# Kernel optimization log

Hardware: AMD Instinct MI355X
Metric: run time of the kernel (lower is better)

The kernel has to match this reference:

```python
import jax, jax.numpy as jnp
import numpy as np

B, S, DD, DE, DA = 32, 2048, 1024, 1024, 1024
NEG = -1000000000.0


def setup_inputs() -> dict:
    key = jax.random.key(0)
    k1, k2, k3, k4, k5 = jax.random.split(key, 5)
    query_state = jax.random.normal(k1, (B, DD), dtype=jnp.float32)
    encoder_hidden_states = jax.random.normal(k2, (B, S, DE), dtype=jnp.float32)
    attention_mask = jax.random.randint(k3, (B, S), 0, 2, dtype=jnp.int32)
    # W_c: Linear(DD+DE -> DA, bias=False): weight shape [DA, DD+DE]
    W_c = jax.random.normal(k4, (DA, DD + DE), dtype=jnp.float32) / np.sqrt(DD + DE)
    # V: Linear(DA -> 1, bias=False): weight shape [1, DA]
    V = jax.random.normal(k5, (1, DA), dtype=jnp.float32) / np.sqrt(DA)
    return {
        "query_state": query_state,
        "encoder_hidden_states": encoder_hidden_states,
        "attention_mask": attention_mask,
        "W_c": W_c,
        "V": V,
    }


def reference(query_state, encoder_hidden_states, attention_mask, W_c, V):
    # Split W_c along input dim: cat([q, e]) @ W_c.T == q @ Wq.T + e @ We.T
    Wq = W_c[:, :DD]          # [DA, DD]
    We = W_c[:, DD:]          # [DA, DE]
    q_proj = jnp.einsum('bd,ad->ba', query_state, Wq)            # [B, DA]
    e_proj = jnp.einsum('bsd,ad->bsa', encoder_hidden_states, We)  # [B, S, DA]
    energies = jnp.tanh(q_proj[:, None, :] + e_proj)             # [B, S, DA]
    scores = jnp.einsum('bsa,a->bs', energies, V[0])             # [B, S]
    scores = jnp.where(attention_mask == 0, NEG, scores)
    attention_weights = jax.nn.softmax(scores, axis=1)           # [B, S]
    context_vector = jnp.einsum('bs,bsd->bd', attention_weights, encoder_hidden_states)
    return context_vector, attention_weights
```

## Files before the change

kernel.cpp:

```cpp
#include <hip/hip_runtime.h>
#include <hip/hip_bf16.h>

#define NB 32
#define NS 2048
#define NDD 1024
#define NDE 1024
#define NDA 1024
#define NEGV (-1000000000.0f)

typedef __attribute__((ext_vector_type(8))) __bf16 bf16x8;
typedef __attribute__((ext_vector_type(4))) float f32x4;

__device__ __forceinline__ float fast_tanh(float x) {
    x = fminf(10.0f, fmaxf(-10.0f, x));
    float e = __expf(2.0f * x);
    return __fdividef(e - 1.0f, e + 1.0f);
}

__device__ __forceinline__ float bfu2f(unsigned short v) {
    union { unsigned u; float f; } c; c.u = (unsigned)v << 16; return c.f;
}

__global__ void prep_we(const float* __restrict__ Wc, __bf16* __restrict__ We) {
    int f = blockIdx.x * 256 + threadIdx.x;
    int a  = f >> 8;
    int k4 = f & 255;
    float4 v = *reinterpret_cast<const float4*>(Wc + (size_t)a * (NDD + NDE) + NDD + k4 * 4);
    union { __bf16 h[4]; uint2 u; } pk;
    pk.h[0] = (__bf16)v.x; pk.h[1] = (__bf16)v.y;
    pk.h[2] = (__bf16)v.z; pk.h[3] = (__bf16)v.w;
    *reinterpret_cast<uint2*>(We + (size_t)a * NDE + k4 * 4) = pk.u;
}

__global__ void prep_e(const float* __restrict__ E, __bf16* __restrict__ Eb) {
    size_t i = ((size_t)blockIdx.x * 256 + threadIdx.x) * 8;
    f32x4 x = __builtin_nontemporal_load(reinterpret_cast<const f32x4*>(E + i));
    f32x4 y = __builtin_nontemporal_load(reinterpret_cast<const f32x4*>(E + i + 4));
    union { __bf16 h[8]; uint4 u; } pk;
    pk.h[0] = (__bf16)x[0]; pk.h[1] = (__bf16)x[1]; pk.h[2] = (__bf16)x[2]; pk.h[3] = (__bf16)x[3];
    pk.h[4] = (__bf16)y[0]; pk.h[5] = (__bf16)y[1]; pk.h[6] = (__bf16)y[2]; pk.h[7] = (__bf16)y[3];
    *reinterpret_cast<uint4*>(Eb + i) = pk.u;
}

__global__ void qproj_kernel(const float* __restrict__ q, const float* __restrict__ Wc,
                             float* __restrict__ qp) {
    __shared__ float qs[NDD];
    int b = blockIdx.y;
    int a = blockIdx.x * 256 + threadIdx.x;
    float4 qv = *reinterpret_cast<const float4*>(q + (size_t)b * NDD + threadIdx.x * 4);
    *reinterpret_cast<float4*>(qs + threadIdx.x * 4) = qv;
    __syncthreads();
    const float* wrow = Wc + (size_t)a * (NDD + NDE);
    float acc = 0.f;
#pragma unroll 4
    for (int k4 = 0; k4 < 256; ++k4) {
        float4 w = *reinterpret_cast<const float4*>(wrow + k4 * 4);
        acc += qs[k4*4+0] * w.x + qs[k4*4+1] * w.y + qs[k4*4+2] * w.z + qs[k4*4+3] * w.w;
    }
    qp[(size_t)b * NDA + a] = acc;
}

__global__ __launch_bounds__(1024, 1) void score256(
    const __bf16* __restrict__ Eb, const __bf16* __restrict__ We,
    const float* __restrict__ qp, const float* __restrict__ Vv,
    float* __restrict__ sp) {
    __shared__ __align__(16) __bf16 As[2][256 * 64];
    __shared__ __align__(16) __bf16 Bs[2][256 * 64];

    const int tid  = threadIdx.x;
    const int lane = tid & 63;
    const int l15  = lane & 15;
    const int h    = lane >> 4;
    const int wid  = tid >> 6;
    const int wr   = wid >> 2;
    const int wc   = wid & 3;

    const int bid = blockIdx.x;
    const int xcd = bid & 7;
    const int j   = bid >> 3;
    const int m   = xcd * 32 + (j >> 2);
    const int n   = j & 3;
    const int row0  = m * 256;
    const int ncol0 = n * 256;
    const int b     = m >> 3;

    f32x4 acc[4][4];
#pragma unroll
    for (int mf = 0; mf < 4; ++mf)
#pragma unroll
        for (int nf = 0; nf < 4; ++nf)
            acc[mf][nf] = (f32x4){0.f, 0.f, 0.f, 0.f};

    int offE[2], offW[2];
#pragma unroll
    for (int i = 0; i < 2; ++i) {
        int chunk = i * 1024 + tid;
        int r  = chunk >> 3;
        int sg = (chunk & 7) ^ (r & 7);
        offE[i] = (row0  + r) * 1024 + sg * 8;
        offW[i] = (ncol0 + r) * 1024 + sg * 8;
    }

    const int slot0 = ((h ^ (l15 & 7)) * 16);
    const int aoffl = (wr * 64 + l15) * 128 + slot0;
    const int boffl = (wc * 64 + l15) * 128 + slot0;

#define STAGE4(abuf, bbuf, kc)                                                          \
    {                                                                                   \
        _Pragma("unroll")                                                               \
        for (int i = 0; i < 2; ++i)                                                     \
            __builtin_amdgcn_global_load_lds(                                           \
                (const __attribute__((address_space(1))) unsigned*)(Eb + offE[i] + (kc)),\
                (__attribute__((address_space(3))) unsigned*)((char*)(abuf) + i * 16384 + wid * 1024), \
                16, 0, 0);                                                              \
        _Pragma("unroll")                                                               \
        for (int i = 0; i < 2; ++i)                                                     \
            __builtin_amdgcn_global_load_lds(                                           \
                (const __attribute__((address_space(1))) unsigned*)(We + offW[i] + (kc)),\
                (__attribute__((address_space(3))) unsigned*)((char*)(bbuf) + i * 16384 + wid * 1024), \
                16, 0, 0);                                                              \
    }

    STAGE4(&As[0][0], &Bs[0][0], 0)
    float qv[4], vv[4];
#pragma unroll
    for (int nf = 0; nf < 4; ++nf) {
        int col = ncol0 + wc * 64 + nf * 16 + l15;
        qv[nf] = qp[(size_t)b * NDA + col];
        vv[nf] = Vv[col];
    }
    __syncthreads();

    for (int T = 0; T < 16; ++T) {
        const int cur = T & 1;
        const char* Ab = (const char*)&As[cur][0];
        const char* Bb = (const char*)&Bs[cur][0];
        if (T < 15) STAGE4(&As[cur ^ 1][0], &Bs[cur ^ 1][0], (T + 1) * 64)

#pragma unroll
        for (int ks = 0; ks < 2; ++ks) {
            bf16x8 bfr[4], afr[4];
#pragma unroll
            for (int nf = 0; nf < 4; ++nf)
                bfr[nf] = *reinterpret_cast<const bf16x8*>(Bb + ((boffl + nf * 2048) ^ (ks * 64)));
#pragma unroll
            for (int mf = 0; mf < 4; ++mf)
                afr[mf] = *reinterpret_cast<const bf16x8*>(Ab + ((aoffl + mf * 2048) ^ (ks * 64)));
            __builtin_amdgcn_s_setprio(1);
#pragma unroll
            for (int mf = 0; mf < 4; ++mf)
#pragma unroll
                for (int nf = 0; nf < 4; ++nf)
                    acc[mf][nf] = __builtin_amdgcn_mfma_f32_16x16x32_bf16(afr[mf], bfr[nf], acc[mf][nf], 0, 0, 0);
            __builtin_amdgcn_s_setprio(0);
        }
        __syncthreads();
    }

    float* ps2 = reinterpret_cast<float*>(&As[0][0]);
#pragma unroll
    for (int mf = 0; mf < 4; ++mf)
#pragma unroll
        for (int jj = 0; jj < 4; ++jj) {
            float s = 0.f;
#pragma unroll
            for (int nf = 0; nf < 4; ++nf)
                s += fast_tanh(qv[nf] + acc[mf][nf][jj]) * vv[nf];
            s += __shfl_xor(s, 1);
            s += __shfl_xor(s, 2);
            s += __shfl_xor(s, 4);
            s += __shfl_xor(s, 8);
            if (l15 == 0)
                ps2[(wr * 64 + mf * 16 + h * 4 + jj) * 4 + wc] = s;
        }
    __syncthreads();
    if (tid < 256)
        sp[(size_t)n * (NB * NS) + row0 + tid] =
            ps2[tid * 4] + ps2[tid * 4 + 1] + ps2[tid * 4 + 2] + ps2[tid * 4 + 3];
}

__global__ void softmax_kernel(const float* __restrict__ sp, const int* __restrict__ mask,
                               float* __restrict__ wout, int np) {
    int b = blockIdx.x;
    const int* mrow = mask + (size_t)b * NS;
    float v[8];
    float lmax = -INFINITY;
#pragma unroll
    for (int jj = 0; jj < 8; ++jj) {
        int s = threadIdx.x + 256 * jj;
        float sc = 0.f;
        for (int nn = 0; nn < np; ++nn) sc += sp[(size_t)nn * (NB * NS) + b * NS + s];
        v[jj] = (mrow[s] == 0) ? NEGV : sc;
        lmax = fmaxf(lmax, v[jj]);
    }
#pragma unroll
    for (int mm = 1; mm <= 32; mm <<= 1) lmax = fmaxf(lmax, __shfl_xor(lmax, mm));
    __shared__ float redm[4], reds[4];
    if ((threadIdx.x & 63) == 0) redm[threadIdx.x >> 6] = lmax;
    __syncthreads();
    float bmax = fmaxf(fmaxf(redm[0], redm[1]), fmaxf(redm[2], redm[3]));
    float lsum = 0.f;
#pragma unroll
    for (int jj = 0; jj < 8; ++jj) { v[jj] = __expf(v[jj] - bmax); lsum += v[jj]; }
#pragma unroll
    for (int mm = 1; mm <= 32; mm <<= 1) lsum += __shfl_xor(lsum, mm);
    if ((threadIdx.x & 63) == 0) reds[threadIdx.x >> 6] = lsum;
    __syncthreads();
    float inv = __fdividef(1.0f, reds[0] + reds[1] + reds[2] + reds[3]);
#pragma unroll
    for (int jj = 0; jj < 8; ++jj) wout[(size_t)b * NS + threadIdx.x + 256 * jj] = v[jj] * inv;
}

__global__ void context_bf16(const __bf16* __restrict__ Eb, const float* __restrict__ w,
                             float* __restrict__ ctx) {
    int b  = blockIdx.x >> 3;
    int dc = blockIdx.x & 7;
    int dg = threadIdx.x & 31;
    int ss = threadIdx.x >> 5;
    const __bf16* base = Eb + (size_t)b * NS * NDE + (size_t)(ss * 256) * NDE + dc * 128 + dg * 4;
    const float* wb = w + (size_t)b * NS + ss * 256;
    float a0 = 0.f, a1 = 0.f, a2 = 0.f, a3 = 0.f;
#pragma unroll 8
    for (int s = 0; s < 256; ++s) {
        float ws = wb[s];
        uint2 u = *reinterpret_cast<const uint2*>(base + (size_t)s * NDE);
        a0 = fmaf(ws, bfu2f((unsigned short)(u.x & 0xffff)), a0);
        a1 = fmaf(ws, bfu2f((unsigned short)(u.x >> 16)), a1);
        a2 = fmaf(ws, bfu2f((unsigned short)(u.y & 0xffff)), a2);
        a3 = fmaf(ws, bfu2f((unsigned short)(u.y >> 16)), a3);
    }
    __shared__ float4 part[256];
    part[threadIdx.x] = make_float4(a0, a1, a2, a3);
    __syncthreads();
    if (threadIdx.x < 32) {
        float4 r = part[threadIdx.x];
#pragma unroll
        for (int k = 1; k < 8; ++k) {
            float4 p = part[threadIdx.x + 32 * k];
            r.x += p.x; r.y += p.y; r.z += p.z; r.w += p.w;
        }
        *reinterpret_cast<float4*>(ctx + (size_t)b * NDD + dc * 128 + threadIdx.x * 4) = r;
    }
}

extern "C" void kernel_launch(void* const* d_in, const int* in_sizes, int n_in,
                              void* d_out, int out_size, void* d_ws, size_t ws_size,
                              hipStream_t stream) {
    const float* query = (const float*)d_in[0];
    const float* enc   = (const float*)d_in[1];
    const int*   mask  = (const int*)d_in[2];
    const float* Wc    = (const float*)d_in[3];
    const float* V     = (const float*)d_in[4];

    float* out = (float*)d_out;
    float* ctx = out;
    float* wts = out + NB * NDD;

    const size_t WE_B = (size_t)NDA * NDE * 2;
    const size_t QP_B = (size_t)NB * NDA * 4;
    const size_t SP_B = (size_t)8 * NB * NS * 4;
    char* ws = (char*)d_ws;
    __bf16* We = (__bf16*)ws;
    float*  qp = (float*)(ws + WE_B);
    float*  sp = (float*)(ws + WE_B + QP_B);
    __bf16* Eb = (__bf16*)(ws + WE_B + QP_B + SP_B);

    hipLaunchKernelGGL(prep_we,      dim3(1024),  dim3(256), 0, stream, Wc, We);
    hipLaunchKernelGGL(qproj_kernel, dim3(4, NB), dim3(256), 0, stream, query, Wc, qp);
    hipLaunchKernelGGL(prep_e,       dim3(32768), dim3(256), 0, stream, enc, Eb);
    hipLaunchKernelGGL(score256,     dim3(1024),  dim3(1024), 0, stream, Eb, We, qp, V, sp);
    hipLaunchKernelGGL(softmax_kernel, dim3(NB),  dim3(256), 0, stream, sp, mask, wts, 4);
    hipLaunchKernelGGL(context_bf16, dim3(256),   dim3(256), 0, stream, Eb, wts, ctx);
}
```

Before: 289.6 us.

## Halve K-tile to 32 and allow two 1024-thread blocks per CU

```diff
diff --git a/kernel.cpp b/kernel.cpp
--- a/kernel.cpp
+++ b/kernel.cpp
@@ -60,12 +60,12 @@
     qp[(size_t)b * NDA + a] = acc;
 }
 
-__global__ __launch_bounds__(1024, 1) void score256(
+__global__ __launch_bounds__(1024, 2) void score256(
     const __bf16* __restrict__ Eb, const __bf16* __restrict__ We,
     const float* __restrict__ qp, const float* __restrict__ Vv,
     float* __restrict__ sp) {
-    __shared__ __align__(16) __bf16 As[2][256 * 64];
-    __shared__ __align__(16) __bf16 Bs[2][256 * 64];
+    __shared__ __align__(16) __bf16 As[2][256 * 32];
+    __shared__ __align__(16) __bf16 Bs[2][256 * 32];
 
     const int tid  = threadIdx.x;
     const int lane = tid & 63;
@@ -91,37 +91,36 @@
         for (int nf = 0; nf < 4; ++nf)
             acc[mf][nf] = (f32x4){0.f, 0.f, 0.f, 0.f};
 
-    int offE[2], offW[2];
-#pragma unroll
-    for (int i = 0; i < 2; ++i) {
-        int chunk = i * 1024 + tid;
-        int r  = chunk >> 3;
-        int sg = (chunk & 7) ^ (r & 7);
-        offE[i] = (row0  + r) * 1024 + sg * 8;
-        offW[i] = (ncol0 + r) * 1024 + sg * 8;
-    }
-
-    const int slot0 = ((h ^ (l15 & 7)) * 16);
-    const int aoffl = (wr * 64 + l15) * 128 + slot0;
-    const int boffl = (wc * 64 + l15) * 128 + slot0;
-
-#define STAGE4(abuf, bbuf, kc)                                                          \
+    const int r_st  = tid >> 2;
+    const int sg_st = (tid & 3) ^ ((r_st >> 1) & 3);
+    const int offE  = (row0  + r_st) * 1024 + sg_st * 8;
+    const int offW  = (ncol0 + r_st) * 1024 + sg_st * 8;
+
+    int aoff[4], boff[4];
+#pragma unroll
+    for (int mf = 0; mf < 4; ++mf) {
+        int r = wr * 64 + mf * 16 + l15;
+        aoff[mf] = r * 64 + ((h ^ ((r >> 1) & 3)) << 4);
+    }
+#pragma unroll
+    for (int nf = 0; nf < 4; ++nf) {
+        int r = wc * 64 + nf * 16 + l15;
+        boff[nf] = r * 64 + ((h ^ ((r >> 1) & 3)) << 4);
+    }
+
+#define STAGE(buf, kc)                                                                  \
     {                                                                                   \
-        _Pragma("unroll")                                                               \
-        for (int i = 0; i < 2; ++i)                                                     \
-            __builtin_amdgcn_global_load_lds(                                           \
-                (const __attribute__((address_space(1))) unsigned*)(Eb + offE[i] + (kc)),\
-                (__attribute__((address_space(3))) unsigned*)((char*)(abuf) + i * 16384 + wid * 1024), \
-                16, 0, 0);                                                              \
-        _Pragma("unroll")                                                               \
-        for (int i = 0; i < 2; ++i)                                                     \
-            __builtin_amdgcn_global_load_lds(                                           \
-                (const __attribute__((address_space(1))) unsigned*)(We + offW[i] + (kc)),\
-                (__attribute__((address_space(3))) unsigned*)((char*)(bbuf) + i * 16384 + wid * 1024), \
-                16, 0, 0);                                                              \
-    }
-
-    STAGE4(&As[0][0], &Bs[0][0], 0)
+        __builtin_amdgcn_global_load_lds(                                               \
+            (const __attribute__((address_space(1))) unsigned*)(Eb + offE + (kc)),      \
+            (__attribute__((address_space(3))) unsigned*)((char*)&As[buf][0] + wid * 1024), \
+            16, 0, 0);                                                                  \
+        __builtin_amdgcn_global_load_lds(                                               \
+            (const __attribute__((address_space(1))) unsigned*)(We + offW + (kc)),      \
+            (__attribute__((address_space(3))) unsigned*)((char*)&Bs[buf][0] + wid * 1024), \
+            16, 0, 0);                                                                  \
+    }
+
+    STAGE(0, 0)
     float qv[4], vv[4];
 #pragma unroll
     for (int nf = 0; nf < 4; ++nf) {
@@ -131,29 +130,26 @@
     }
     __syncthreads();
 
-    for (int T = 0; T < 16; ++T) {
+    for (int T = 0; T < 32; ++T) {
         const int cur = T & 1;
         const char* Ab = (const char*)&As[cur][0];
         const char* Bb = (const char*)&Bs[cur][0];
-        if (T < 15) STAGE4(&As[cur ^ 1][0], &Bs[cur ^ 1][0], (T + 1) * 64)
-
-#pragma unroll
-        for (int ks = 0; ks < 2; ++ks) {
-            bf16x8 bfr[4], afr[4];
+        if (T < 31) STAGE(cur ^ 1, (T + 1) * 32)
+
+        bf16x8 afr[4], bfr[4];
+#pragma unroll
+        for (int nf = 0; nf < 4; ++nf)
+            bfr[nf] = *reinterpret_cast<const bf16x8*>(Bb + boff[nf]);
+#pragma unroll
+        for (int mf = 0; mf < 4; ++mf)
+            afr[mf] = *reinterpret_cast<const bf16x8*>(Ab + aoff[mf]);
+        __builtin_amdgcn_s_setprio(1);
+#pragma unroll
+        for (int mf = 0; mf < 4; ++mf)
 #pragma unroll
             for (int nf = 0; nf < 4; ++nf)
-                bfr[nf] = *reinterpret_cast<const bf16x8*>(Bb + ((boffl + nf * 2048) ^ (ks * 64)));
-#pragma unroll
-            for (int mf = 0; mf < 4; ++mf)
-                afr[mf] = *reinterpret_cast<const bf16x8*>(Ab + ((aoffl + mf * 2048) ^ (ks * 64)));
-            __builtin_amdgcn_s_setprio(1);
-#pragma unroll
-            for (int mf = 0; mf < 4; ++mf)
-#pragma unroll
-                for (int nf = 0; nf < 4; ++nf)
-                    acc[mf][nf] = __builtin_amdgcn_mfma_f32_16x16x32_bf16(afr[mf], bfr[nf], acc[mf][nf], 0, 0, 0);
-            __builtin_amdgcn_s_setprio(0);
-        }
+                acc[mf][nf] = __builtin_amdgcn_mfma_f32_16x16x32_bf16(afr[mf], bfr[nf], acc[mf][nf], 0, 0, 0);
+        __builtin_amdgcn_s_setprio(0);
         __syncthreads();
     }
 
```

Measured after the change: 295.3 us. Within noise of the previous version (+2.0%).
